# Kernel tuning notes

Hardware: AMD Instinct MI355X
Metric: run time of the kernel (lower is better)

The kernel has to match this reference:

```python
import jax, jax.numpy as jnp
import numpy as np

H = 100  # hidden size

def _lstm_layer(x, Wih, Whh, b):
    # x: [B, T, D_in]; Wih: [4H, D_in]; Whh: [4H, H]; b: [4H]
    # Precompute input contribution for all timesteps (batched GEMM).
    xw = jnp.einsum('btd,gd->btg', x, Wih) + b            # [B, T, 4H]
    B = x.shape[0]
    h0 = jnp.zeros((B, H), x.dtype)
    c0 = jnp.zeros((B, H), x.dtype)
    WhhT = Whh.T                                          # [H, 4H]

    def step(carry, xw_t):
        h, c = carry
        gates = xw_t + h @ WhhT                           # [B, 4H]
        i, f, g, o = jnp.split(gates, 4, axis=-1)         # PyTorch order i,f,g,o
        i = jax.nn.sigmoid(i)
        f = jax.nn.sigmoid(f)
        g = jnp.tanh(g)
        o = jax.nn.sigmoid(o)
        c = f * c + i * g
        h = o * jnp.tanh(c)
        return (h, c), h

    _, hs = jax.lax.scan(step, (h0, c0), jnp.swapaxes(xw, 0, 1))  # [T, B, H]
    return jnp.swapaxes(hs, 0, 1)                         # [B, T, H]


def setup_inputs() -> dict:
    key = jax.random.key(0)
    ks = jax.random.split(key, 12)
    B, T = 512, 512
    s = 0.08  # small init scale to avoid gate saturation
    return {
        'z':    jax.random.normal(ks[0], (B, T, 1), jnp.float32),
        'Wih0': jax.random.normal(ks[1], (4 * H, 1), jnp.float32) * s,
        'Whh0': jax.random.normal(ks[2], (4 * H, H), jnp.float32) * s,
        'b0':   jax.random.normal(ks[3], (4 * H,), jnp.float32) * s,
        'Wih1': jax.random.normal(ks[4], (4 * H, H), jnp.float32) * s,
        'Whh1': jax.random.normal(ks[5], (4 * H, H), jnp.float32) * s,
        'b1':   jax.random.normal(ks[6], (4 * H,), jnp.float32) * s,
        'Wih2': jax.random.normal(ks[7], (4 * H, H), jnp.float32) * s,
        'Whh2': jax.random.normal(ks[8], (4 * H, H), jnp.float32) * s,
        'b2':   jax.random.normal(ks[9], (4 * H,), jnp.float32) * s,
        'Wp':   jax.random.normal(ks[10], (1, H), jnp.float32) * s,
        'bp':   jax.random.normal(ks[11], (1,), jnp.float32) * s,
    }


def reference(z, Wih0, Whh0, b0, Wih1, Whh1, b1, Wih2, Whh2, b2, Wp, bp):
    h = _lstm_layer(z, Wih0, Whh0, b0)
    h = _lstm_layer(h, Wih1, Whh1, b1)
    h = _lstm_layer(h, Wih2, Whh2, b2)       # [B, T, H]
    return jnp.tanh(jnp.einsum('bth,oh->bto', h, Wp) + bp)  # [B, T, 1]
```

## Files before the change

### kernel.cpp

```cpp
#include <hip/hip_runtime.h>
#include <cstdint>
#include <cstddef>


#define HH 100
#define G4 400
#define NB 512
#define NT 512

__device__ __forceinline__ float sigm(float x) {
  return 1.0f / (1.0f + __expf(-x));
}
__device__ __forceinline__ float tanh_(float x) {
  return 1.0f - 2.0f / (__expf(2.0f * x) + 1.0f);
}
__device__ __forceinline__ float qb1(float v) {
  return __int_as_float(__builtin_amdgcn_ds_swizzle(__float_as_int(v), 0x8055));
}
__device__ __forceinline__ float qb2(float v) {
  return __int_as_float(__builtin_amdgcn_ds_swizzle(__float_as_int(v), 0x80AA));
}
__device__ __forceinline__ float qb3(float v) {
  return __int_as_float(__builtin_amdgcn_ds_swizzle(__float_as_int(v), 0x80FF));
}

__global__ __attribute__((amdgpu_flat_work_group_size(512, 512),
                          amdgpu_waves_per_eu(2, 2)))
void lstm_layer12(
    const float* x,
    const float* __restrict__ Wih,
    const float* __restrict__ Whh,
    const float* __restrict__ bias,
    float* hseq)
{
  const int b = blockIdx.x;
  const int tid = threadIdx.x;

  __shared__ __align__(16) float h_dbuf[2][HH];
  __shared__ __align__(16) float x_dbuf[2][HH];

  const bool isG = tid < G4;
  const int u = tid >> 2, g = tid & 3;
  const int row = g * HH + u;

  float whh[HH], wih[HH];
  float bb = 0.0f, c = 0.0f;
  if (isG) {
    const float4* wh4 = reinterpret_cast<const float4*>(Whh + (size_t)row * HH);
    const float4* wi4 = reinterpret_cast<const float4*>(Wih + (size_t)row * HH);
#pragma unroll
    for (int k = 0; k < HH / 4; ++k) {
      float4 a = wh4[k];
      whh[4 * k] = a.x; whh[4 * k + 1] = a.y; whh[4 * k + 2] = a.z; whh[4 * k + 3] = a.w;
      float4 bq = wi4[k];
      wih[4 * k] = bq.x; wih[4 * k + 1] = bq.y; wih[4 * k + 2] = bq.z; wih[4 * k + 3] = bq.w;
    }
    bb = bias[row];
  }
  if (tid < HH) h_dbuf[0][tid] = 0.0f;

  const float* xb = x + (size_t)b * NT * HH;
  float* hb = hseq + (size_t)b * NT * HH;

  const unsigned pf = (unsigned)(tid - 448);
  if (pf < 25u) {
    reinterpret_cast<float4*>(x_dbuf[0])[pf] =
        reinterpret_cast<const float4*>(xb)[pf];
  }
  __syncthreads();

  for (int t = 0; t < NT; ++t) {
    const int cur = t & 1, nxt = cur ^ 1;

    if (pf < 25u) {
      int tt = (t + 1 < NT) ? t + 1 : NT - 1;
      reinterpret_cast<float4*>(x_dbuf[nxt])[pf] =
          reinterpret_cast<const float4*>(xb + (size_t)tt * HH)[pf];
    }

    if (isG) {
      float a0 = 0.f, a1 = 0.f, a2 = 0.f, a3 = 0.f;
      const float4* x4 = reinterpret_cast<const float4*>(x_dbuf[cur]);
      const float4* h4 = reinterpret_cast<const float4*>(h_dbuf[cur]);
#pragma unroll
      for (int k = 0; k < HH / 4; ++k) {
        float4 v = x4[k];
        a0 += v.x * wih[4 * k];     a1 += v.y * wih[4 * k + 1];
        a2 += v.z * wih[4 * k + 2]; a3 += v.w * wih[4 * k + 3];
      }
#pragma unroll
      for (int k = 0; k < HH / 4; ++k) {
        float4 v = h4[k];
        a0 += v.x * whh[4 * k];     a1 += v.y * whh[4 * k + 1];
        a2 += v.z * whh[4 * k + 2]; a3 += v.w * whh[4 * k + 3];
      }
      float acc = bb + ((a0 + a1) + (a2 + a3));
      float act = (g == 2) ? tanh_(acc) : sigm(acc);
      float fv = qb1(act);
      float gv = qb2(act);
      float ov = qb3(act);
      if (g == 0) {
        c = fv * c + act * gv;
        float hv = ov * tanh_(c);
        h_dbuf[nxt][u] = hv;
        hb[(size_t)t * HH + u] = hv;
      }
    }
    __syncthreads();
  }
}

__global__ __attribute__((amdgpu_flat_work_group_size(512, 512),
                          amdgpu_waves_per_eu(4, 4)))
void lstm_layer0(
    const float* __restrict__ z,
    const float* __restrict__ Wih,
    const float* __restrict__ Whh,
    const float* __restrict__ bias,
    float* __restrict__ hseq)
{
  const int b = blockIdx.x;
  const int tid = threadIdx.x;

  __shared__ __align__(16) float h_dbuf[2][HH];

  const bool isG = tid < G4;
  const int u = tid >> 2, g = tid & 3;
  const int row = g * HH + u;

  float w[HH];
  float w0 = 0.f, bb = 0.f, c = 0.f;
  if (isG) {
    const float4* w4 = reinterpret_cast<const float4*>(Whh + (size_t)row * HH);
#pragma unroll
    for (int k = 0; k < HH / 4; ++k) {
      float4 v = w4[k];
      w[4 * k] = v.x; w[4 * k + 1] = v.y; w[4 * k + 2] = v.z; w[4 * k + 3] = v.w;
    }
    w0 = Wih[row];
    bb = bias[row];
  }
  if (tid < HH) h_dbuf[0][tid] = 0.0f;

  const float* zb = z + (size_t)b * NT;
  float* hb = hseq + (size_t)b * NT * HH;

  float zc = zb[0];
  __syncthreads();

  for (int t = 0; t < NT; ++t) {
    const int cur = t & 1, nxt = cur ^ 1;
    float zn = (t + 1 < NT) ? zb[t + 1] : 0.f;

    if (isG) {
      float a0 = 0.f, a1 = 0.f, a2 = 0.f, a3 = 0.f;
      const float4* h4 = reinterpret_cast<const float4*>(h_dbuf[cur]);
#pragma unroll
      for (int k = 0; k < HH / 4; ++k) {
        float4 v = h4[k];
        a0 += v.x * w[4 * k];     a1 += v.y * w[4 * k + 1];
        a2 += v.z * w[4 * k + 2]; a3 += v.w * w[4 * k + 3];
      }
      float acc = bb + w0 * zc + ((a0 + a1) + (a2 + a3));
      float act = (g == 2) ? tanh_(acc) : sigm(acc);
      float fv = qb1(act);
      float gv = qb2(act);
      float ov = qb3(act);
      if (g == 0) {
        c = fv * c + act * gv;
        float hv = ov * tanh_(c);
        h_dbuf[nxt][u] = hv;
        hb[(size_t)t * HH + u] = hv;
      }
    }
    zc = zn;
    __syncthreads();
  }
}

__global__ __launch_bounds__(256) void proj_kernel(
    const float* __restrict__ hseq,
    const float* __restrict__ Wp,
    const float* __restrict__ bp,
    float* __restrict__ out)
{
  int idx = blockIdx.x * blockDim.x + threadIdx.x;
  if (idx >= NB * NT) return;
  const float4* h4 = reinterpret_cast<const float4*>(hseq + (size_t)idx * HH);
  const float4* w4 = reinterpret_cast<const float4*>(Wp);
  float a0 = 0.f, a1 = 0.f, a2 = 0.f, a3 = 0.f;
#pragma unroll
  for (int k = 0; k < HH / 4; ++k) {
    float4 h = h4[k];
    float4 w = w4[k];
    a0 += h.x * w.x; a1 += h.y * w.y; a2 += h.z * w.z; a3 += h.w * w.w;
  }
  out[idx] = tanh_(((a0 + a1) + (a2 + a3)) + bp[0]);
}

extern "C" void kernel_launch(void* const* d_in, const int* in_sizes, int n_in,
                              void* d_out, int out_size, void* d_ws, size_t ws_size,
                              hipStream_t stream) {
  const float* z    = (const float*)d_in[0];
  const float* Wih0 = (const float*)d_in[1];
  const float* Whh0 = (const float*)d_in[2];
  const float* b0   = (const float*)d_in[3];
  const float* Wih1 = (const float*)d_in[4];
  const float* Whh1 = (const float*)d_in[5];
  const float* b1   = (const float*)d_in[6];
  const float* Wih2 = (const float*)d_in[7];
  const float* Whh2 = (const float*)d_in[8];
  const float* b2   = (const float*)d_in[9];
  const float* Wp   = (const float*)d_in[10];
  const float* bp   = (const float*)d_in[11];
  float* out = (float*)d_out;

  float* hbuf = (float*)d_ws;

  lstm_layer0<<<NB, 512, 0, stream>>>(z, Wih0, Whh0, b0, hbuf);
  lstm_layer12<<<NB, 512, 0, stream>>>(hbuf, Wih1, Whh1, b1, hbuf);
  lstm_layer12<<<NB, 512, 0, stream>>>(hbuf, Wih2, Whh2, b2, hbuf);
  proj_kernel<<<(NB * NT + 255) / 256, 256, 0, stream>>>(hbuf, Wp, bp, out);
}
```

Before: 3.027 ms.

## Tile LSTM time steps and batch input projection per tile into LDS

Merges the layer-0 and layer-1/2 kernels into one templated kernel that processes time in tiles of 8 steps. For each tile it loads the inputs into LDS and computes the input-to-gate projection for all 8 steps up front, streaming Wih from global memory instead of keeping it in registers. The recurrent loop then adds only the precomputed value. This halves weight register pressure and takes the input GEMV off the serial critical path, at the cost of re-reading Wih from global/L2 every tile and adding barriers.

```diff
diff --git a/kernel.cpp b/kernel.cpp
--- a/kernel.cpp
+++ b/kernel.cpp
@@ -7,6 +7,7 @@
 #define G4 400
 #define NB 512
 #define NT 512
+#define TT 8
 
 __device__ __forceinline__ float sigm(float x) {
   return 1.0f / (1.0f + __expf(-x));
@@ -24,9 +25,8 @@
   return __int_as_float(__builtin_amdgcn_ds_swizzle(__float_as_int(v), 0x80FF));
 }
 
-__global__ __attribute__((amdgpu_flat_work_group_size(512, 512),
-                          amdgpu_waves_per_eu(2, 2)))
-void lstm_layer12(
+template <int K>
+__global__ __launch_bounds__(512, 2) void lstm_tiled(
     const float* x,
     const float* __restrict__ Wih,
     const float* __restrict__ Whh,
@@ -36,145 +36,89 @@
   const int b = blockIdx.x;
   const int tid = threadIdx.x;
 
-  __shared__ __align__(16) float h_dbuf[2][HH];
-  __shared__ __align__(16) float x_dbuf[2][HH];
-
-  const bool isG = tid < G4;
-  const int u = tid >> 2, g = tid & 3;
-  const int row = g * HH + u;
-
-  float whh[HH], wih[HH];
-  float bb = 0.0f, c = 0.0f;
-  if (isG) {
-    const float4* wh4 = reinterpret_cast<const float4*>(Whh + (size_t)row * HH);
-    const float4* wi4 = reinterpret_cast<const float4*>(Wih + (size_t)row * HH);
-#pragma unroll
-    for (int k = 0; k < HH / 4; ++k) {
-      float4 a = wh4[k];
-      whh[4 * k] = a.x; whh[4 * k + 1] = a.y; whh[4 * k + 2] = a.z; whh[4 * k + 3] = a.w;
-      float4 bq = wi4[k];
-      wih[4 * k] = bq.x; wih[4 * k + 1] = bq.y; wih[4 * k + 2] = bq.z; wih[4 * k + 3] = bq.w;
-    }
-    bb = bias[row];
-  }
-  if (tid < HH) h_dbuf[0][tid] = 0.0f;
-
-  const float* xb = x + (size_t)b * NT * HH;
-  float* hb = hseq + (size_t)b * NT * HH;
-
-  const unsigned pf = (unsigned)(tid - 448);
-  if (pf < 25u) {
-    reinterpret_cast<float4*>(x_dbuf[0])[pf] =
-        reinterpret_cast<const float4*>(xb)[pf];
-  }
-  __syncthreads();
-
-  for (int t = 0; t < NT; ++t) {
-    const int cur = t & 1, nxt = cur ^ 1;
-
-    if (pf < 25u) {
-      int tt = (t + 1 < NT) ? t + 1 : NT - 1;
-      reinterpret_cast<float4*>(x_dbuf[nxt])[pf] =
-          reinterpret_cast<const float4*>(xb + (size_t)tt * HH)[pf];
-    }
-
-    if (isG) {
-      float a0 = 0.f, a1 = 0.f, a2 = 0.f, a3 = 0.f;
-      const float4* x4 = reinterpret_cast<const float4*>(x_dbuf[cur]);
-      const float4* h4 = reinterpret_cast<const float4*>(h_dbuf[cur]);
-#pragma unroll
-      for (int k = 0; k < HH / 4; ++k) {
-        float4 v = x4[k];
-        a0 += v.x * wih[4 * k];     a1 += v.y * wih[4 * k + 1];
-        a2 += v.z * wih[4 * k + 2]; a3 += v.w * wih[4 * k + 3];
-      }
-#pragma unroll
-      for (int k = 0; k < HH / 4; ++k) {
-        float4 v = h4[k];
-        a0 += v.x * whh[4 * k];     a1 += v.y * whh[4 * k + 1];
-        a2 += v.z * whh[4 * k + 2]; a3 += v.w * whh[4 * k + 3];
-      }
-      float acc = bb + ((a0 + a1) + (a2 + a3));
-      float act = (g == 2) ? tanh_(acc) : sigm(acc);
-      float fv = qb1(act);
-      float gv = qb2(act);
-      float ov = qb3(act);
-      if (g == 0) {
-        c = fv * c + act * gv;
-        float hv = ov * tanh_(c);
-        h_dbuf[nxt][u] = hv;
-        hb[(size_t)t * HH + u] = hv;
-      }
-    }
-    __syncthreads();
-  }
-}
-
-__global__ __attribute__((amdgpu_flat_work_group_size(512, 512),
-                          amdgpu_waves_per_eu(4, 4)))
-void lstm_layer0(
-    const float* __restrict__ z,
-    const float* __restrict__ Wih,
-    const float* __restrict__ Whh,
-    const float* __restrict__ bias,
-    float* __restrict__ hseq)
-{
-  const int b = blockIdx.x;
-  const int tid = threadIdx.x;
-
+  __shared__ __align__(16) float xw_lds[TT * G4];
+  __shared__ __align__(16) float x_lds[TT * K];
   __shared__ __align__(16) float h_dbuf[2][HH];
 
   const bool isG = tid < G4;
   const int u = tid >> 2, g = tid & 3;
   const int row = g * HH + u;
 
-  float w[HH];
-  float w0 = 0.f, bb = 0.f, c = 0.f;
+  float4 whh4[HH / 4];
+  float bb = 0.0f, c = 0.0f, wih1 = 0.0f;
   if (isG) {
     const float4* w4 = reinterpret_cast<const float4*>(Whh + (size_t)row * HH);
 #pragma unroll
-    for (int k = 0; k < HH / 4; ++k) {
-      float4 v = w4[k];
-      w[4 * k] = v.x; w[4 * k + 1] = v.y; w[4 * k + 2] = v.z; w[4 * k + 3] = v.w;
-    }
-    w0 = Wih[row];
+    for (int k = 0; k < HH / 4; ++k) whh4[k] = w4[k];
     bb = bias[row];
+    if constexpr (K == 1) wih1 = Wih[row];
   }
   if (tid < HH) h_dbuf[0][tid] = 0.0f;
 
-  const float* zb = z + (size_t)b * NT;
+  const float* xb = x + (size_t)b * NT * K;
   float* hb = hseq + (size_t)b * NT * HH;
-
-  float zc = zb[0];
   __syncthreads();
 
-  for (int t = 0; t < NT; ++t) {
-    const int cur = t & 1, nxt = cur ^ 1;
-    float zn = (t + 1 < NT) ? zb[t + 1] : 0.f;
+  for (int tile = 0; tile < NT / TT; ++tile) {
+    const int t0 = tile * TT;
+
+    {
+      const float4* src = reinterpret_cast<const float4*>(xb + (size_t)t0 * K);
+      float4* dst = reinterpret_cast<float4*>(x_lds);
+      for (int i = tid; i < (TT * K) / 4; i += 512) dst[i] = src[i];
+    }
+    __syncthreads();
 
     if (isG) {
-      float a0 = 0.f, a1 = 0.f, a2 = 0.f, a3 = 0.f;
-      const float4* h4 = reinterpret_cast<const float4*>(h_dbuf[cur]);
+      float acc[TT];
 #pragma unroll
-      for (int k = 0; k < HH / 4; ++k) {
-        float4 v = h4[k];
-        a0 += v.x * w[4 * k];     a1 += v.y * w[4 * k + 1];
-        a2 += v.z * w[4 * k + 2]; a3 += v.w * w[4 * k + 3];
+      for (int tt = 0; tt < TT; ++tt) acc[tt] = bb;
+      if constexpr (K == 1) {
+#pragma unroll
+        for (int tt = 0; tt < TT; ++tt) acc[tt] += wih1 * x_lds[tt];
+      } else {
+        const float4* wi4 = reinterpret_cast<const float4*>(Wih + (size_t)row * K);
+#pragma unroll
+        for (int k4 = 0; k4 < K / 4; ++k4) {
+          float4 w = wi4[k4];
+#pragma unroll
+          for (int tt = 0; tt < TT; ++tt) {
+            const float* xr = x_lds + tt * K + 4 * k4;
+            acc[tt] += w.x * xr[0] + w.y * xr[1] + w.z * xr[2] + w.w * xr[3];
+          }
+        }
       }
-      float acc = bb + w0 * zc + ((a0 + a1) + (a2 + a3));
-      float act = (g == 2) ? tanh_(acc) : sigm(acc);
-      float fv = qb1(act);
-      float gv = qb2(act);
-      float ov = qb3(act);
-      if (g == 0) {
-        c = fv * c + act * gv;
-        float hv = ov * tanh_(c);
-        h_dbuf[nxt][u] = hv;
-        hb[(size_t)t * HH + u] = hv;
+#pragma unroll
+      for (int tt = 0; tt < TT; ++tt) xw_lds[tt * G4 + tid] = acc[tt];
+    }
+    __syncthreads();
+
+    for (int s = 0; s < TT; ++s) {
+      const int cur = s & 1, nxt = cur ^ 1;
+      if (isG) {
+        float xa = xw_lds[s * G4 + tid];
+        float a0 = 0.f, a1 = 0.f, a2 = 0.f, a3 = 0.f;
+        const float4* h4 = reinterpret_cast<const float4*>(h_dbuf[cur]);
+#pragma unroll
+        for (int k = 0; k < HH / 4; ++k) {
+          float4 v = h4[k];
+          a0 += v.x * whh4[k].x; a1 += v.y * whh4[k].y;
+          a2 += v.z * whh4[k].z; a3 += v.w * whh4[k].w;
+        }
+        float accv = xa + ((a0 + a1) + (a2 + a3));
+        float act = (g == 2) ? tanh_(accv) : sigm(accv);
+        float fv = qb1(act);
+        float gv = qb2(act);
+        float ov = qb3(act);
+        if (g == 0) {
+          c = fv * c + act * gv;
+          float hv = ov * tanh_(c);
+          h_dbuf[nxt][u] = hv;
+          hb[(size_t)(t0 + s) * HH + u] = hv;
+        }
       }
+      __syncthreads();
     }
-    zc = zn;
-    __syncthreads();
   }
 }
 
@@ -217,8 +161,8 @@
 
   float* hbuf = (float*)d_ws;
 
-  lstm_layer0<<<NB, 512, 0, stream>>>(z, Wih0, Whh0, b0, hbuf);
-  lstm_layer12<<<NB, 512, 0, stream>>>(hbuf, Wih1, Whh1, b1, hbuf);
-  lstm_layer12<<<NB, 512, 0, stream>>>(hbuf, Wih2, Whh2, b2, hbuf);
+  lstm_tiled<1><<<NB, 512, 0, stream>>>(z, Wih0, Whh0, b0, hbuf);
+  lstm_tiled<HH><<<NB, 512, 0, stream>>>(hbuf, Wih1, Whh1, b1, hbuf);
+  lstm_tiled<HH><<<NB, 512, 0, stream>>>(hbuf, Wih2, Whh2, b2, hbuf);
   proj_kernel<<<(NB * NT + 255) / 256, 256, 0, stream>>>(hbuf, Wp, bp, out);
 }
```

Result: slower. 4.527 ms (+49.6%).

## Split layers 1-2 into chunked input GEMM plus Whh-only recurrence

Applied to the files above, without the earlier changes.

Layers 1 and 2 now run as time chunks. For each chunk, an xw_gemm kernel precomputes the input projection plus bias into workspace, then a templated lstm_rec kernel runs the recurrence with only Whh held in registers. Hidden and cell state carry across chunks through hseq and a new cbuf. Layer 0 uses the same template with the scalar z input. Dropping Wih from registers is meant to let two 512-thread blocks fit per CU, so all batch blocks are resident at once, at the cost of extra launches and the workspace traffic for xw. If the workspace is too small it falls back to the old fused kernel.

```diff
diff --git a/kernel.cpp b/kernel.cpp
--- a/kernel.cpp
+++ b/kernel.cpp
@@ -24,9 +24,155 @@
   return __int_as_float(__builtin_amdgcn_ds_swizzle(__float_as_int(v), 0x80FF));
 }
 
-__global__ __attribute__((amdgpu_flat_work_group_size(512, 512),
-                          amdgpu_waves_per_eu(2, 2)))
-void lstm_layer12(
+template <int MODE>
+__global__ __launch_bounds__(512, 2) void lstm_rec(
+    const float* __restrict__ xsrc,
+    const float* __restrict__ Wih,
+    const float* __restrict__ Whh,
+    const float* __restrict__ bias,
+    float* __restrict__ hseq,
+    float* __restrict__ cbuf,
+    int t0, int tlen)
+{
+  const int b = blockIdx.x;
+  const int tid = threadIdx.x;
+
+  __shared__ __align__(16) float h_lds[2][HH];
+
+  const bool isG = tid < G4;
+  const int u = tid >> 2, g = tid & 3;
+  const int row = g * HH + u;
+
+  float4 whh4[HH / 4];
+  float bb = 0.f, c = 0.f, wih1 = 0.f;
+  if (isG) {
+    const float4* w4 = reinterpret_cast<const float4*>(Whh + (size_t)row * HH);
+#pragma unroll
+    for (int k = 0; k < HH / 4; ++k) whh4[k] = w4[k];
+    if constexpr (MODE == 1) {
+      wih1 = Wih[row];
+      bb = bias[row];
+    }
+  }
+
+  if (t0 == 0) {
+    if (tid < HH) h_lds[0][tid] = 0.0f;
+  } else {
+    if (tid < HH) h_lds[0][tid] = hseq[((size_t)b * NT + (t0 - 1)) * HH + tid];
+    if (isG && g == 0) c = cbuf[b * HH + u];
+  }
+
+  const float* xwb = xsrc + (size_t)b * tlen * G4;
+  const float* zb  = xsrc + (size_t)b * NT;
+  float* hb = hseq + (size_t)b * NT * HH;
+
+  float xa_n = 0.f, zc = 0.f;
+  if constexpr (MODE == 0) {
+    if (isG) xa_n = xwb[tid];
+  } else {
+    zc = zb[t0];
+  }
+  __syncthreads();
+
+  for (int s = 0; s < tlen; ++s) {
+    const int cur = s & 1, nxt = cur ^ 1;
+
+    float xa = 0.f, zn = 0.f;
+    if constexpr (MODE == 0) {
+      xa = xa_n;
+      if (isG) {
+        int sn = (s + 1 < tlen) ? s + 1 : tlen - 1;
+        xa_n = xwb[(size_t)sn * G4 + tid];
+      }
+    } else {
+      int tn = (t0 + s + 1 < NT) ? t0 + s + 1 : NT - 1;
+      zn = zb[tn];
+    }
+
+    if (isG) {
+      float a0 = 0.f, a1 = 0.f, a2 = 0.f, a3 = 0.f;
+      const float4* h4 = reinterpret_cast<const float4*>(h_lds[cur]);
+#pragma unroll
+      for (int k = 0; k < HH / 4; ++k) {
+        float4 v = h4[k];
+        a0 += v.x * whh4[k].x; a1 += v.y * whh4[k].y;
+        a2 += v.z * whh4[k].z; a3 += v.w * whh4[k].w;
+      }
+      float acc = xa + ((a0 + a1) + (a2 + a3));
+      if constexpr (MODE == 1) acc += bb + wih1 * zc;
+      float act = (g == 2) ? tanh_(acc) : sigm(acc);
+      float fv = qb1(act);
+      float gv = qb2(act);
+      float ov = qb3(act);
+      if (g == 0) {
+        c = fv * c + act * gv;
+        float hv = ov * tanh_(c);
+        h_lds[nxt][u] = hv;
+        hb[(size_t)(t0 + s) * HH + u] = hv;
+      }
+    }
+    if constexpr (MODE == 1) zc = zn;
+    __syncthreads();
+  }
+
+  if (isG && g == 0) cbuf[b * HH + u] = c;
+}
+
+__global__ __launch_bounds__(512, 2) void xw_gemm(
+    const float* __restrict__ hsrc,
+    const float* __restrict__ Wih,
+    const float* __restrict__ bias,
+    float* __restrict__ xw,
+    int t0, int tlen)
+{
+  const int b = blockIdx.x;
+  const int tid = threadIdx.x;
+
+  __shared__ __align__(16) float x_lds[32 * HH];
+
+  const bool isG = tid < G4;
+  const int u = tid >> 2, g = tid & 3;
+  const int row = g * HH + u;
+
+  float4 wih4[HH / 4];
+  float bb = 0.f;
+  if (isG) {
+    const float4* w4 = reinterpret_cast<const float4*>(Wih + (size_t)row * HH);
+#pragma unroll
+    for (int k = 0; k < HH / 4; ++k) wih4[k] = w4[k];
+    bb = bias[row];
+  }
+
+  const float* hsb = hsrc + ((size_t)b * NT + t0) * HH;
+  float* xwb = xw + (size_t)b * tlen * G4;
+
+  for (int tt0 = 0; tt0 < tlen; tt0 += 32) {
+    const int S = (tlen - tt0 < 32) ? (tlen - tt0) : 32;
+    __syncthreads();
+    {
+      const float4* src = reinterpret_cast<const float4*>(hsb + (size_t)tt0 * HH);
+      float4* dst = reinterpret_cast<float4*>(x_lds);
+      const int n4 = S * HH / 4;
+      for (int i = tid; i < n4; i += 512) dst[i] = src[i];
+    }
+    __syncthreads();
+    if (isG) {
+      for (int tt = 0; tt < S; ++tt) {
+        const float4* xr = reinterpret_cast<const float4*>(x_lds + tt * HH);
+        float a0 = 0.f, a1 = 0.f, a2 = 0.f, a3 = 0.f;
+#pragma unroll
+        for (int k = 0; k < HH / 4; ++k) {
+          float4 v = xr[k];
+          a0 += v.x * wih4[k].x; a1 += v.y * wih4[k].y;
+          a2 += v.z * wih4[k].z; a3 += v.w * wih4[k].w;
+        }
+        xwb[(size_t)(tt0 + tt) * G4 + tid] = bb + ((a0 + a1) + (a2 + a3));
+      }
+    }
+  }
+}
+
+__global__ __launch_bounds__(512, 2) void lstm_fused(
     const float* x,
     const float* __restrict__ Wih,
     const float* __restrict__ Whh,
@@ -35,16 +181,13 @@
 {
   const int b = blockIdx.x;
   const int tid = threadIdx.x;
-
   __shared__ __align__(16) float h_dbuf[2][HH];
   __shared__ __align__(16) float x_dbuf[2][HH];
-
   const bool isG = tid < G4;
   const int u = tid >> 2, g = tid & 3;
   const int row = g * HH + u;
-
   float whh[HH], wih[HH];
-  float bb = 0.0f, c = 0.0f;
+  float bb = 0.f, c = 0.f;
   if (isG) {
     const float4* wh4 = reinterpret_cast<const float4*>(Whh + (size_t)row * HH);
     const float4* wi4 = reinterpret_cast<const float4*>(Wih + (size_t)row * HH);
@@ -58,26 +201,19 @@
     bb = bias[row];
   }
   if (tid < HH) h_dbuf[0][tid] = 0.0f;
-
   const float* xb = x + (size_t)b * NT * HH;
   float* hb = hseq + (size_t)b * NT * HH;
-
   const unsigned pf = (unsigned)(tid - 448);
-  if (pf < 25u) {
-    reinterpret_cast<float4*>(x_dbuf[0])[pf] =
-        reinterpret_cast<const float4*>(xb)[pf];
-  }
+  if (pf < 25u)
+    reinterpret_cast<float4*>(x_dbuf[0])[pf] = reinterpret_cast<const float4*>(xb)[pf];
   __syncthreads();
-
   for (int t = 0; t < NT; ++t) {
     const int cur = t & 1, nxt = cur ^ 1;
-
     if (pf < 25u) {
       int tt = (t + 1 < NT) ? t + 1 : NT - 1;
       reinterpret_cast<float4*>(x_dbuf[nxt])[pf] =
           reinterpret_cast<const float4*>(xb + (size_t)tt * HH)[pf];
     }
-
     if (isG) {
       float a0 = 0.f, a1 = 0.f, a2 = 0.f, a3 = 0.f;
       const float4* x4 = reinterpret_cast<const float4*>(x_dbuf[cur]);
@@ -106,74 +242,6 @@
         hb[(size_t)t * HH + u] = hv;
       }
     }
-    __syncthreads();
-  }
-}
-
-__global__ __attribute__((amdgpu_flat_work_group_size(512, 512),
-                          amdgpu_waves_per_eu(4, 4)))
-void lstm_layer0(
-    const float* __restrict__ z,
-    const float* __restrict__ Wih,
-    const float* __restrict__ Whh,
-    const float* __restrict__ bias,
-    float* __restrict__ hseq)
-{
-  const int b = blockIdx.x;
-  const int tid = threadIdx.x;
-
-  __shared__ __align__(16) float h_dbuf[2][HH];
-
-  const bool isG = tid < G4;
-  const int u = tid >> 2, g = tid & 3;
-  const int row = g * HH + u;
-
-  float w[HH];
-  float w0 = 0.f, bb = 0.f, c = 0.f;
-  if (isG) {
-    const float4* w4 = reinterpret_cast<const float4*>(Whh + (size_t)row * HH);
-#pragma unroll
-    for (int k = 0; k < HH / 4; ++k) {
-      float4 v = w4[k];
-      w[4 * k] = v.x; w[4 * k + 1] = v.y; w[4 * k + 2] = v.z; w[4 * k + 3] = v.w;
-    }
-    w0 = Wih[row];
-    bb = bias[row];
-  }
-  if (tid < HH) h_dbuf[0][tid] = 0.0f;
-
-  const float* zb = z + (size_t)b * NT;
-  float* hb = hseq + (size_t)b * NT * HH;
-
-  float zc = zb[0];
-  __syncthreads();
-
-  for (int t = 0; t < NT; ++t) {
-    const int cur = t & 1, nxt = cur ^ 1;
-    float zn = (t + 1 < NT) ? zb[t + 1] : 0.f;
-
-    if (isG) {
-      float a0 = 0.f, a1 = 0.f, a2 = 0.f, a3 = 0.f;
-      const float4* h4 = reinterpret_cast<const float4*>(h_dbuf[cur]);
-#pragma unroll
-      for (int k = 0; k < HH / 4; ++k) {
-        float4 v = h4[k];
-        a0 += v.x * w[4 * k];     a1 += v.y * w[4 * k + 1];
-        a2 += v.z * w[4 * k + 2]; a3 += v.w * w[4 * k + 3];
-      }
-      float acc = bb + w0 * zc + ((a0 + a1) + (a2 + a3));
-      float act = (g == 2) ? tanh_(acc) : sigm(acc);
-      float fv = qb1(act);
-      float gv = qb2(act);
-      float ov = qb3(act);
-      if (g == 0) {
-        c = fv * c + act * gv;
-        float hv = ov * tanh_(c);
-        h_dbuf[nxt][u] = hv;
-        hb[(size_t)t * HH + u] = hv;
-      }
-    }
-    zc = zn;
     __syncthreads();
   }
 }
@@ -216,9 +284,33 @@
   float* out = (float*)d_out;
 
   float* hbuf = (float*)d_ws;
-
-  lstm_layer0<<<NB, 512, 0, stream>>>(z, Wih0, Whh0, b0, hbuf);
-  lstm_layer12<<<NB, 512, 0, stream>>>(hbuf, Wih1, Whh1, b1, hbuf);
-  lstm_layer12<<<NB, 512, 0, stream>>>(hbuf, Wih2, Whh2, b2, hbuf);
+  float* cbuf = hbuf + (size_t)NB * NT * HH;
+  float* xwb  = cbuf + (size_t)NB * HH;
+
+  const size_t base_bytes = ((size_t)NB * NT * HH + (size_t)NB * HH) * 4;
+  int CT = 0;
+  for (int c : {128, 64, 32, 16, 8}) {
+    if (base_bytes + (size_t)NB * c * G4 * 4 <= ws_size) { CT = c; break; }
+  }
+
+  lstm_rec<1><<<NB, 512, 0, stream>>>(z, Wih0, Whh0, b0, hbuf, cbuf, 0, NT);
+
+  const float* WihL[2] = {Wih1, Wih2};
+  const float* WhhL[2] = {Whh1, Whh2};
+  const float* bL[2]   = {b1, b2};
+
+  if (CT > 0) {
+    for (int l = 0; l < 2; ++l) {
+      for (int t0 = 0; t0 < NT; t0 += CT) {
+        xw_gemm<<<NB, 512, 0, stream>>>(hbuf, WihL[l], bL[l], xwb, t0, CT);
+        lstm_rec<0><<<NB, 512, 0, stream>>>(xwb, WihL[l], WhhL[l], bL[l],
+                                            hbuf, cbuf, t0, CT);
+      }
+    }
+  } else {
+    lstm_fused<<<NB, 512, 0, stream>>>(hbuf, Wih1, Whh1, b1, hbuf);
+    lstm_fused<<<NB, 512, 0, stream>>>(hbuf, Wih2, Whh2, b2, hbuf);
+  }
+
   proj_kernel<<<(NB * NT + 255) / 256, 256, 0, stream>>>(hbuf, Wp, bp, out);
 }
```

Measured after the change: 6.146 ms. +103.0%, slower.
